# Kernel optimization log

Measured on AMD Instinct MI355X. Metric: run time of the kernel, lower is better.

Reference implementation:

```python
import jax, jax.numpy as jnp
import numpy as np

MARGIN = 1.0


def setup_inputs() -> dict:
    key = jax.random.key(0)
    k1, k2, k3 = jax.random.split(key, 3)
    B, D, C = 16384, 256, 2000
    pred_embedding = jax.random.normal(k1, (B, D), dtype=jnp.float32)
    batch_label = jax.random.randint(k2, (B,), 0, C, dtype=jnp.int64)
    train_classes = jnp.arange(C, dtype=jnp.int64)
    train_sig = jax.random.normal(k3, (D, C), dtype=jnp.float32)
    return {
        "pred_embedding": pred_embedding,
        "batch_label": batch_label,
        "train_classes": train_classes,
        "train_sig": train_sig,
    }


def reference(pred_embedding, batch_label, train_classes, train_sig):
    # scores[j, k] = <pred_embedding[j], train_sig[:, train_classes[k]]>
    # Single GEMM replaces the per-pair dot-product loops.
    sig_cols = train_sig[:, train_classes]            # [D, C]
    scores = jnp.einsum("bd,dc->bc", pred_embedding, sig_cols)  # [B, C]
    # ground-truth class score per row: <XW_j, train_sig[:, y_j]>
    gt = jnp.einsum("bd,db->b", pred_embedding, train_sig[:, batch_label])  # [B]
    # exclude the class equal to the row label
    mask = (train_classes[None, :] != batch_label[:, None])  # [B, C] bool
    hinge = jnp.maximum(MARGIN + scores - gt[:, None], 0.0)
    loss = jnp.sum(jnp.where(mask, hinge, 0.0))
    return loss
```

## Files before the change

### kernel.cpp

```cpp
#include <hip/hip_runtime.h>

#define B_SZ 16384
#define D_SZ 256
#define C_SZ 2000
#define C_PAD 2048
#define MARGIN_F 1.0f
#define NBLK 1024

typedef __bf16 bf16x8 __attribute__((ext_vector_type(8)));
typedef __bf16 bf16x4 __attribute__((ext_vector_type(4)));
typedef float floatx16 __attribute__((ext_vector_type(16)));

__device__ inline void gld_lds16(const void* g, void* l) {
  __builtin_amdgcn_global_load_lds(
      (const __attribute__((address_space(1))) void*)g,
      (__attribute__((address_space(3))) void*)l, 16, 0, 0);
}


__global__ __launch_bounds__(256) void sigf_kernel(
    const float* __restrict__ sig, __bf16* __restrict__ sigf,
    unsigned int* __restrict__ cnt) {
  if (blockIdx.x == 0 && threadIdx.x == 0) *cnt = 0u;
  int ct = (int)blockIdx.x;
#pragma unroll
  for (int it = 0; it < 4; it++) {
    int ch = it * 256 + threadIdx.x;
    int lane = ch & 63, ks = ch >> 6;
    int col = ct * 32 + (lane & 31);
    int kb = ks * 16 + (lane >> 5) * 8;
    bf16x8 o;
    if (col < C_SZ) {
#pragma unroll
      for (int j = 0; j < 8; j++) o[j] = (__bf16)sig[(size_t)(kb + j) * C_SZ + col];
    } else {
#pragma unroll
      for (int j = 0; j < 8; j++) o[j] = (__bf16)0.f;
    }
    *(bf16x8*)(sigf + ((size_t)(ct * 16 + ks) * 64 + lane) * 8) = o;
  }
}

__global__ __launch_bounds__(256) void prep_kernel(
    const float* __restrict__ pred, const __bf16* __restrict__ sigf,
    const int* __restrict__ label, __bf16* __restrict__ predf,
    float* __restrict__ gt) {
  __shared__ float ldsP[32][257];
  int bid = (int)blockIdx.x;
  int tid = threadIdx.x;
#pragma unroll
  for (int it = 0; it < 8; it++) {
    int idx = it * 1024 + tid * 4;
    int r = idx >> 8, c = idx & 255;
    float4 v = *(const float4*)(pred + (size_t)(bid * 32 + r) * D_SZ + c);
    ldsP[r][c] = v.x; ldsP[r][c + 1] = v.y;
    ldsP[r][c + 2] = v.z; ldsP[r][c + 3] = v.w;
  }
  __syncthreads();
#pragma unroll
  for (int it = 0; it < 4; it++) {
    int ch = it * 256 + tid;
    int lane = ch & 63, ks = ch >> 6;
    int r = lane & 31, kb = ks * 16 + (lane >> 5) * 8;
    bf16x8 o;
#pragma unroll
    for (int j = 0; j < 8; j++) o[j] = (__bf16)ldsP[r][kb + j];
    *(bf16x8*)(predf + ((size_t)(bid * 16 + ks) * 64 + lane) * 8) = o;
  }
  int lane = tid & 63, w = tid >> 6;
  for (int rr = 0; rr < 8; rr++) {
    int r = w * 8 + rr;
    int row = bid * 32 + r;
    int lbl = label[row];
    int tile = lbl >> 5, l5 = lbl & 31;
    int k0 = lane * 4;
    int ks = k0 >> 4;
    int kh = (k0 >> 3) & 1;
    int j0 = k0 & 7;
    bf16x4 sb = *(const bf16x4*)(sigf +
        (((size_t)(tile * 16 + ks) * 64) + kh * 32 + l5) * 8 + j0);
    float s = 0.f;
#pragma unroll
    for (int i = 0; i < 4; i++)
      s += (float)(__bf16)ldsP[r][k0 + i] * (float)sb[i];
#pragma unroll
    for (int off = 32; off > 0; off >>= 1) s += __shfl_down(s, off, 64);
    if (lane == 0) gt[row] = s;
  }
}

__global__ __launch_bounds__(256, 2) void mfma_fused_kernel(
    const __bf16* __restrict__ predf, const __bf16* __restrict__ sigf,
    const float* __restrict__ gt, float* __restrict__ partial,
    unsigned int* __restrict__ cnt, float* __restrict__ out) {
  __shared__ __bf16 Bs[4096 * 8];
  __shared__ float red[4];
  __shared__ float lastFlag;
  int tid = threadIdx.x;
  int lane = tid & 63;
  int w = tid >> 6;
  int kh = lane >> 5, lm = lane & 31;
  int bid = (int)blockIdx.x;
  int i = bid >> 3;
  int rsb = (bid & 7) * 8 + (i & 7);
  int cg = i >> 3;

#pragma unroll
  for (int s = 0; s < 16; s++) {
    int q0 = s * 256 + w * 64;
    gld_lds16(sigf + ((size_t)cg * 4096 + q0 + lane) * 8, (void*)(Bs + (size_t)q0 * 8));
  }

  bf16x8 afr[2][16];
#pragma unroll
  for (int rt = 0; rt < 2; rt++)
#pragma unroll
    for (int ks = 0; ks < 16; ks++)
      afr[rt][ks] = *(const bf16x8*)(predf +
          (((size_t)(rsb * 8 + w * 2 + rt) * 16 + ks) * 64 + lane) * 8);

  float mgv[2][16];
#pragma unroll
  for (int rt = 0; rt < 2; rt++)
#pragma unroll
    for (int reg = 0; reg < 16; reg++) {
      int row = rsb * 256 + w * 64 + rt * 32 + (reg & 3) + 8 * (reg >> 2) + 4 * kh;
      mgv[rt][reg] = MARGIN_F - gt[row];
    }
  __syncthreads();

  float sum = 0.f;
  for (int ct = 0; ct < 4; ct++) {
    floatx16 acc0 = {}, acc1 = {};
#pragma unroll
    for (int ks = 0; ks < 16; ks++) {
      bf16x8 bfr = *(const bf16x8*)(Bs + (size_t)((ct * 16 + ks) * 64 + lane) * 8);
      acc0 = __builtin_amdgcn_mfma_f32_32x32x16_bf16(afr[0][ks], bfr, acc0, 0, 0, 0);
      acc1 = __builtin_amdgcn_mfma_f32_32x32x16_bf16(afr[1][ks], bfr, acc1, 0, 0, 0);
    }
    int col = cg * 128 + ct * 32 + lm;
    float keep = (col < C_SZ) ? 1.f : 0.f;
#pragma unroll
    for (int reg = 0; reg < 16; reg++) {
      sum += keep * fmaxf(acc0[reg] + mgv[0][reg], 0.f);
      sum += keep * fmaxf(acc1[reg] + mgv[1][reg], 0.f);
    }
  }
#pragma unroll
  for (int off = 32; off > 0; off >>= 1) sum += __shfl_down(sum, off, 64);
  if (lane == 0) red[w] = sum;
  __syncthreads();
  if (tid == 0) {
    partial[bid] = red[0] + red[1] + red[2] + red[3];
    __threadfence();
    unsigned int old = atomicAdd(cnt, 1u);
    lastFlag = (old == NBLK - 1) ? 1.f : 0.f;
  }
  __syncthreads();
  if (lastFlag != 0.f) {
    float s = (tid == 0) ? -(float)B_SZ * MARGIN_F : 0.f;
    for (int p = tid; p < NBLK; p += 256)
      s += atomicAdd(&partial[p], 0.f);
#pragma unroll
    for (int off = 32; off > 0; off >>= 1) s += __shfl_down(s, off, 64);
    if (lane == 0) red[w] = s;
    __syncthreads();
    if (tid == 0) out[0] = red[0] + red[1] + red[2] + red[3];
  }
}

extern "C" void kernel_launch(void* const* d_in, const int* in_sizes, int n_in,
                              void* d_out, int out_size, void* d_ws, size_t ws_size,
                              hipStream_t stream) {
  const float* pred  = (const float*)d_in[0];
  const int*   label = (const int*)d_in[1];
  const float* sig   = (const float*)d_in[3];
  float* out = (float*)d_out;

  float*        gt      = (float*)d_ws;
  float*        partial = (float*)((char*)d_ws + (64 << 10));
  unsigned int* cnt     = (unsigned int*)((char*)d_ws + (68 << 10));
  __bf16*       predf   = (__bf16*)((char*)d_ws + (128 << 10));
  __bf16*       sigf    = (__bf16*)((char*)d_ws + (128 << 10) + (8 << 20));

  sigf_kernel<<<64, 256, 0, stream>>>(sig, sigf, cnt);
  prep_kernel<<<512, 256, 0, stream>>>(pred, sigf, label, predf, gt);
  mfma_fused_kernel<<<NBLK, 256, 0, stream>>>(predf, sigf, gt, partial, cnt, out);
}
```

Before: 114.2 us.

## Merge prep kernels and retile GEMM to smaller tiles with atomic accumulators

The two preprocessing kernels are merged into one launch. Their blocks now split between converting pred (and computing gt straight from the fp32 sig) and converting sig into the MFMA fragment layout, which removes one launch and the dependency between the two. The main kernel is retiled: 4096 blocks each handle 64 rows by 128 columns, with A staged in LDS and B held in registers. This uses less LDS and asks for 3 blocks per CU. Per-block partial sums go through atomics into 64 slots rather than a 1024-entry array, which shortens the final reduction but adds atomic contention and more blocks doing redundant loads.

```diff
diff --git a/kernel.cpp b/kernel.cpp
--- a/kernel.cpp
+++ b/kernel.cpp
@@ -5,10 +5,9 @@
 #define C_SZ 2000
 #define C_PAD 2048
 #define MARGIN_F 1.0f
-#define NBLK 1024
+#define GBLK 4096
 
 typedef __bf16 bf16x8 __attribute__((ext_vector_type(8)));
-typedef __bf16 bf16x4 __attribute__((ext_vector_type(4)));
 typedef float floatx16 __attribute__((ext_vector_type(16)));
 
 __device__ inline void gld_lds16(const void* g, void* l) {
@@ -18,154 +17,139 @@
 }
 
 
-__global__ __launch_bounds__(256) void sigf_kernel(
-    const float* __restrict__ sig, __bf16* __restrict__ sigf,
-    unsigned int* __restrict__ cnt) {
-  if (blockIdx.x == 0 && threadIdx.x == 0) *cnt = 0u;
-  int ct = (int)blockIdx.x;
+__global__ __launch_bounds__(256) void prep_kernel(
+    const float* __restrict__ pred, const float* __restrict__ sig,
+    const int* __restrict__ label, __bf16* __restrict__ predf,
+    __bf16* __restrict__ sigf, float* __restrict__ gt,
+    float* __restrict__ accs, unsigned int* __restrict__ cnt) {
+  int bid = (int)blockIdx.x;
+  int tid = threadIdx.x;
+  if (bid < 512) {
+    __shared__ float ldsP[32][260];
 #pragma unroll
-  for (int it = 0; it < 4; it++) {
-    int ch = it * 256 + threadIdx.x;
-    int lane = ch & 63, ks = ch >> 6;
-    int col = ct * 32 + (lane & 31);
-    int kb = ks * 16 + (lane >> 5) * 8;
-    bf16x8 o;
-    if (col < C_SZ) {
+    for (int it = 0; it < 8; it++) {
+      int idx = it * 1024 + tid * 4;
+      int r = idx >> 8, c = idx & 255;
+      float4 v = *(const float4*)(pred + (size_t)(bid * 32 + r) * D_SZ + c);
+      *(float4*)&ldsP[r][c] = v;
+    }
+    __syncthreads();
 #pragma unroll
-      for (int j = 0; j < 8; j++) o[j] = (__bf16)sig[(size_t)(kb + j) * C_SZ + col];
-    } else {
+    for (int it = 0; it < 4; it++) {
+      int ch = it * 256 + tid;
+      int lane = ch & 63, ks = ch >> 6;
+      int r = lane & 31, kb = ks * 16 + (lane >> 5) * 8;
+      float4 u0 = *(const float4*)&ldsP[r][kb];
+      float4 u1 = *(const float4*)&ldsP[r][kb + 4];
+      bf16x8 o;
+      o[0] = (__bf16)u0.x; o[1] = (__bf16)u0.y; o[2] = (__bf16)u0.z; o[3] = (__bf16)u0.w;
+      o[4] = (__bf16)u1.x; o[5] = (__bf16)u1.y; o[6] = (__bf16)u1.z; o[7] = (__bf16)u1.w;
+      *(bf16x8*)(predf + ((size_t)(bid * 16 + ks) * 64 + lane) * 8) = o;
+    }
+    int lane = tid & 63, w = tid >> 6;
+    for (int rr = 0; rr < 8; rr++) {
+      int r = w * 8 + rr;
+      int row = bid * 32 + r;
+      int lbl = label[row];
+      float4 pq = *(const float4*)&ldsP[r][lane * 4];
+      float pv[4] = {pq.x, pq.y, pq.z, pq.w};
+      float s = 0.f;
 #pragma unroll
-      for (int j = 0; j < 8; j++) o[j] = (__bf16)0.f;
+      for (int i = 0; i < 4; i++)
+        s += (float)(__bf16)pv[i] * (float)(__bf16)sig[(size_t)(lane * 4 + i) * C_SZ + lbl];
+#pragma unroll
+      for (int off = 32; off > 0; off >>= 1) s += __shfl_down(s, off, 64);
+      if (lane == 0) gt[row] = s;
     }
-    *(bf16x8*)(sigf + ((size_t)(ct * 16 + ks) * 64 + lane) * 8) = o;
+  } else {
+    if (bid == 512 && tid < 65) {
+      if (tid < 64) accs[tid] = 0.f; else *cnt = 0u;
+    }
+    int ct = bid - 512;
+#pragma unroll
+    for (int it = 0; it < 4; it++) {
+      int ch = it * 256 + tid;
+      int lane = ch & 63, ks = ch >> 6;
+      int col = ct * 32 + (lane & 31);
+      int kb = ks * 16 + (lane >> 5) * 8;
+      bf16x8 o;
+      if (col < C_SZ) {
+#pragma unroll
+        for (int j = 0; j < 8; j++) o[j] = (__bf16)sig[(size_t)(kb + j) * C_SZ + col];
+      } else {
+#pragma unroll
+        for (int j = 0; j < 8; j++) o[j] = (__bf16)0.f;
+      }
+      *(bf16x8*)(sigf + ((size_t)(ct * 16 + ks) * 64 + lane) * 8) = o;
+    }
   }
 }
 
-__global__ __launch_bounds__(256) void prep_kernel(
-    const float* __restrict__ pred, const __bf16* __restrict__ sigf,
-    const int* __restrict__ label, __bf16* __restrict__ predf,
-    float* __restrict__ gt) {
-  __shared__ float ldsP[32][257];
-  int bid = (int)blockIdx.x;
-  int tid = threadIdx.x;
-#pragma unroll
-  for (int it = 0; it < 8; it++) {
-    int idx = it * 1024 + tid * 4;
-    int r = idx >> 8, c = idx & 255;
-    float4 v = *(const float4*)(pred + (size_t)(bid * 32 + r) * D_SZ + c);
-    ldsP[r][c] = v.x; ldsP[r][c + 1] = v.y;
-    ldsP[r][c + 2] = v.z; ldsP[r][c + 3] = v.w;
-  }
-  __syncthreads();
-#pragma unroll
-  for (int it = 0; it < 4; it++) {
-    int ch = it * 256 + tid;
-    int lane = ch & 63, ks = ch >> 6;
-    int r = lane & 31, kb = ks * 16 + (lane >> 5) * 8;
-    bf16x8 o;
-#pragma unroll
-    for (int j = 0; j < 8; j++) o[j] = (__bf16)ldsP[r][kb + j];
-    *(bf16x8*)(predf + ((size_t)(bid * 16 + ks) * 64 + lane) * 8) = o;
-  }
-  int lane = tid & 63, w = tid >> 6;
-  for (int rr = 0; rr < 8; rr++) {
-    int r = w * 8 + rr;
-    int row = bid * 32 + r;
-    int lbl = label[row];
-    int tile = lbl >> 5, l5 = lbl & 31;
-    int k0 = lane * 4;
-    int ks = k0 >> 4;
-    int kh = (k0 >> 3) & 1;
-    int j0 = k0 & 7;
-    bf16x4 sb = *(const bf16x4*)(sigf +
-        (((size_t)(tile * 16 + ks) * 64) + kh * 32 + l5) * 8 + j0);
-    float s = 0.f;
-#pragma unroll
-    for (int i = 0; i < 4; i++)
-      s += (float)(__bf16)ldsP[r][k0 + i] * (float)sb[i];
-#pragma unroll
-    for (int off = 32; off > 0; off >>= 1) s += __shfl_down(s, off, 64);
-    if (lane == 0) gt[row] = s;
-  }
-}
-
-__global__ __launch_bounds__(256, 2) void mfma_fused_kernel(
+__global__ __launch_bounds__(256, 3) void mfma_fused_kernel(
     const __bf16* __restrict__ predf, const __bf16* __restrict__ sigf,
-    const float* __restrict__ gt, float* __restrict__ partial,
+    const float* __restrict__ gt, float* __restrict__ accs,
     unsigned int* __restrict__ cnt, float* __restrict__ out) {
-  __shared__ __bf16 Bs[4096 * 8];
+  __shared__ __bf16 As[2048 * 8];
+  __shared__ float gtS[64];
   __shared__ float red[4];
-  __shared__ float lastFlag;
+  __shared__ unsigned int lastFlag;
   int tid = threadIdx.x;
   int lane = tid & 63;
   int w = tid >> 6;
   int kh = lane >> 5, lm = lane & 31;
   int bid = (int)blockIdx.x;
-  int i = bid >> 3;
-  int rsb = (bid & 7) * 8 + (i & 7);
-  int cg = i >> 3;
+  int rsb = (bid & 7) * 32 + ((bid >> 3) & 31);
+  int cg = bid >> 8;
 
 #pragma unroll
-  for (int s = 0; s < 16; s++) {
-    int q0 = s * 256 + w * 64;
-    gld_lds16(sigf + ((size_t)cg * 4096 + q0 + lane) * 8, (void*)(Bs + (size_t)q0 * 8));
+  for (int t = 0; t < 8; t++) {
+    int q0 = w * 512 + t * 64;
+    gld_lds16(predf + ((size_t)rsb * 2048 + q0 + lane) * 8, (void*)(As + (size_t)q0 * 8));
+  }
+  if (tid < 64) gtS[tid] = gt[rsb * 64 + tid];
+
+  bf16x8 bfrg[16];
+#pragma unroll
+  for (int ks = 0; ks < 16; ks++)
+    bfrg[ks] = *(const bf16x8*)(sigf + (((size_t)(cg * 4 + w) * 16 + ks) * 64 + lane) * 8);
+  __syncthreads();
+
+  floatx16 acc[2] = {};
+#pragma unroll
+  for (int ks = 0; ks < 16; ks++) {
+#pragma unroll
+    for (int rt = 0; rt < 2; rt++) {
+      bf16x8 a = *(const bf16x8*)(As + (size_t)((rt * 16 + ks) * 64 + lane) * 8);
+      acc[rt] = __builtin_amdgcn_mfma_f32_32x32x16_bf16(a, bfrg[ks], acc[rt], 0, 0, 0);
+    }
   }
 
-  bf16x8 afr[2][16];
-#pragma unroll
-  for (int rt = 0; rt < 2; rt++)
-#pragma unroll
-    for (int ks = 0; ks < 16; ks++)
-      afr[rt][ks] = *(const bf16x8*)(predf +
-          (((size_t)(rsb * 8 + w * 2 + rt) * 16 + ks) * 64 + lane) * 8);
-
-  float mgv[2][16];
+  int col = cg * 128 + w * 32 + lm;
+  float keep = (col < C_SZ) ? 1.f : 0.f;
+  float sum = 0.f;
 #pragma unroll
   for (int rt = 0; rt < 2; rt++)
 #pragma unroll
     for (int reg = 0; reg < 16; reg++) {
-      int row = rsb * 256 + w * 64 + rt * 32 + (reg & 3) + 8 * (reg >> 2) + 4 * kh;
-      mgv[rt][reg] = MARGIN_F - gt[row];
+      int rl = rt * 32 + (reg & 3) + 8 * (reg >> 2) + 4 * kh;
+      sum += keep * fmaxf(acc[rt][reg] + MARGIN_F - gtS[rl], 0.f);
     }
-  __syncthreads();
-
-  float sum = 0.f;
-  for (int ct = 0; ct < 4; ct++) {
-    floatx16 acc0 = {}, acc1 = {};
-#pragma unroll
-    for (int ks = 0; ks < 16; ks++) {
-      bf16x8 bfr = *(const bf16x8*)(Bs + (size_t)((ct * 16 + ks) * 64 + lane) * 8);
-      acc0 = __builtin_amdgcn_mfma_f32_32x32x16_bf16(afr[0][ks], bfr, acc0, 0, 0, 0);
-      acc1 = __builtin_amdgcn_mfma_f32_32x32x16_bf16(afr[1][ks], bfr, acc1, 0, 0, 0);
-    }
-    int col = cg * 128 + ct * 32 + lm;
-    float keep = (col < C_SZ) ? 1.f : 0.f;
-#pragma unroll
-    for (int reg = 0; reg < 16; reg++) {
-      sum += keep * fmaxf(acc0[reg] + mgv[0][reg], 0.f);
-      sum += keep * fmaxf(acc1[reg] + mgv[1][reg], 0.f);
-    }
-  }
 #pragma unroll
   for (int off = 32; off > 0; off >>= 1) sum += __shfl_down(sum, off, 64);
   if (lane == 0) red[w] = sum;
   __syncthreads();
   if (tid == 0) {
-    partial[bid] = red[0] + red[1] + red[2] + red[3];
+    atomicAdd(&accs[bid & 63], red[0] + red[1] + red[2] + red[3]);
     __threadfence();
     unsigned int old = atomicAdd(cnt, 1u);
-    lastFlag = (old == NBLK - 1) ? 1.f : 0.f;
+    lastFlag = (old == GBLK - 1) ? 1u : 0u;
   }
   __syncthreads();
-  if (lastFlag != 0.f) {
-    float s = (tid == 0) ? -(float)B_SZ * MARGIN_F : 0.f;
-    for (int p = tid; p < NBLK; p += 256)
-      s += atomicAdd(&partial[p], 0.f);
+  if (lastFlag && tid < 64) {
+    float s = atomicAdd(&accs[tid], 0.f);
 #pragma unroll
     for (int off = 32; off > 0; off >>= 1) s += __shfl_down(s, off, 64);
-    if (lane == 0) red[w] = s;
-    __syncthreads();
-    if (tid == 0) out[0] = red[0] + red[1] + red[2] + red[3];
+    if (tid == 0) out[0] = s - (float)B_SZ * MARGIN_F;
   }
 }
 
@@ -177,13 +161,12 @@
   const float* sig   = (const float*)d_in[3];
   float* out = (float*)d_out;
 
-  float*        gt      = (float*)d_ws;
-  float*        partial = (float*)((char*)d_ws + (64 << 10));
-  unsigned int* cnt     = (unsigned int*)((char*)d_ws + (68 << 10));
-  __bf16*       predf   = (__bf16*)((char*)d_ws + (128 << 10));
-  __bf16*       sigf    = (__bf16*)((char*)d_ws + (128 << 10) + (8 << 20));
+  float*        gt    = (float*)d_ws;
+  float*        accs  = (float*)((char*)d_ws + (64 << 10));
+  unsigned int* cnt   = (unsigned int*)((char*)d_ws + (66 << 10));
+  __bf16*       predf = (__bf16*)((char*)d_ws + (128 << 10));
+  __bf16*       sigf  = (__bf16*)((char*)d_ws + (128 << 10) + (8 << 20));
 
-  sigf_kernel<<<64, 256, 0, stream>>>(sig, sigf, cnt);
-  prep_kernel<<<512, 256, 0, stream>>>(pred, sigf, label, predf, gt);
-  mfma_fused_kernel<<<NBLK, 256, 0, stream>>>(predf, sigf, gt, partial, cnt, out);
+  prep_kernel<<<576, 256, 0, stream>>>(pred, sig, label, predf, sigf, gt, accs, cnt);
+  mfma_fused_kernel<<<GBLK, 256, 0, stream>>>(predf, sigf, gt, accs, cnt, out);
 }
```

After: 189.1 us. +65.6%, slower.
